# Performance work log

Measured on AMD Instinct MI355X. Metric: run time of the kernel, lower is better.

The kernel has to match this reference:

```python
import jax, jax.numpy as jnp
import numpy as np

B, N, E, C_IN, C_OUT = 16, 4096, 131072, 256, 256


def setup_inputs() -> dict:
    key = jax.random.key(0)
    k1, k2, k3, k4 = jax.random.split(key, 4)
    x = jax.random.normal(k1, (B, N, C_IN), dtype=jnp.float32)
    edge_index = jax.random.randint(k2, (B, 2, E), 0, N, dtype=jnp.int32)
    edge_weight = jax.random.uniform(k3, (B, E), dtype=jnp.float32)
    # glorot init for weight [C_in, C_out]
    scale = float(np.sqrt(6.0 / (C_IN + C_OUT)))
    W = jax.random.uniform(k4, (C_IN, C_OUT), dtype=jnp.float32, minval=-scale, maxval=scale)
    return {"x": x, "edge_index": edge_index, "edge_weight": edge_weight, "W": W}


def _gcn_one_graph(xi, ei, ewi, W):
    # xi: [N, C_in], ei: [2, E+N], ewi: [E+N]
    n = xi.shape[0]
    row, col = ei[0], ei[1]
    deg = jax.ops.segment_sum(ewi, row, num_segments=n)            # [N]
    deg_inv = jnp.where(deg > 0, jax.lax.rsqrt(deg), 0.0)          # deg^-0.5, inf -> 0
    norm = deg_inv[row] * ewi * deg_inv[col]                       # [E+N]
    xw = xi @ W                                                    # [N, C_out]
    msg = norm[:, None] * xw[col]                                  # gather + scale
    out = jax.ops.segment_sum(msg, row, num_segments=n)            # scatter-add to rows
    return jax.nn.relu(out)                                        # act = F.relu, bias=False


def reference(x, edge_index, edge_weight, W):
    b, n, _ = x.shape
    # add self loops with weight 1 (fill_value=1)
    loop = jnp.arange(n, dtype=edge_index.dtype)
    loop_idx = jnp.broadcast_to(jnp.stack([loop, loop])[None], (b, 2, n))
    ei = jnp.concatenate([edge_index, loop_idx], axis=-1)          # [B, 2, E+N]
    ew = jnp.concatenate([edge_weight, jnp.ones((b, n), x.dtype)], axis=-1)  # [B, E+N]
    return jax.vmap(_gcn_one_graph, in_axes=(0, 0, 0, None))(x, ei, ew, W)
```

## Files before the change

kernel.cpp:

```cpp
#include <hip/hip_runtime.h>
#include <cstdint>
#include <cstddef>

#define BB 16
#define NN 4096
#define EE 131072
#define CIN 256
#define COUT 256
#define NCH 16
#define CHE (EE / NCH)

typedef __attribute__((ext_vector_type(8))) _Float16 h16x8;
typedef __attribute__((ext_vector_type(4))) float f32x4;

#define GLDS16(g, l) __builtin_amdgcn_global_load_lds( \
    (const __attribute__((address_space(1))) uint32_t*)(g), \
    (__attribute__((address_space(3))) uint32_t*)(l), 16, 0, 0)

__global__ __launch_bounds__(256) void phaseA_kernel(const float* __restrict__ x, _Float16* __restrict__ xh,
                                                     const float* __restrict__ W, _Float16* __restrict__ wt,
                                                     const int* __restrict__ ei, const float* __restrict__ ew,
                                                     int* __restrict__ chist, float* __restrict__ wdeg) {
    __shared__ int h[NN];
    __shared__ float wh[NN];
    int bid = blockIdx.x;
    int tid = threadIdx.x;
    if (bid < BB * NCH) {
        int b = bid >> 4, c = bid & (NCH - 1);
        for (int i = tid; i < NN; i += 256) { h[i] = 0; wh[i] = 0.f; }
        __syncthreads();
        const int* rows = ei + (size_t)b * 2 * EE + (size_t)c * CHE;
        const float* w = ew + (size_t)b * EE + (size_t)c * CHE;
        #pragma unroll 4
        for (int j = 0; j < CHE / 256; ++j) {
            int row = rows[j * 256 + tid];
            float wv = w[j * 256 + tid];
            atomicAdd(&h[row], 1);
            atomicAdd(&wh[row], wv);
        }
        __syncthreads();
        int* co = chist + ((size_t)b * NCH + c) * NN;
        float* wo = wdeg + ((size_t)b * NCH + c) * NN;
        for (int i = tid; i < NN; i += 256) { co[i] = h[i]; wo[i] = wh[i]; }
    } else if (bid < BB * NCH + (BB * NN * CIN) / (256 * 8)) {
        size_t u = (size_t)(bid - BB * NCH) * 256 + tid;
        const float* g = &x[u * 8];
        float4 f0 = *reinterpret_cast<const float4*>(g);
        float4 f1 = *reinterpret_cast<const float4*>(g + 4);
        h16x8 v;
        v[0] = (_Float16)f0.x; v[1] = (_Float16)f0.y; v[2] = (_Float16)f0.z; v[3] = (_Float16)f0.w;
        v[4] = (_Float16)f1.x; v[5] = (_Float16)f1.y; v[6] = (_Float16)f1.z; v[7] = (_Float16)f1.w;
        *reinterpret_cast<h16x8*>(&xh[u * 8]) = v;
    } else {
        int n = bid - (BB * NCH + (BB * NN * CIN) / (256 * 8));
        int k = tid;
        wt[n * CIN + k] = (_Float16)W[(size_t)k * COUT + n];
    }
}

__global__ __launch_bounds__(1024) void scanfused_kernel(const int* __restrict__ chist, const float* __restrict__ wdeg,
                                                         int* __restrict__ chunkbase, int* __restrict__ roff,
                                                         float* __restrict__ dinv) {
    int b = blockIdx.x, tid = threadIdx.x;
    int wid = tid >> 6, lane = tid & 63;
    __shared__ int wsum[16];
    __shared__ int wbase[16];
    __shared__ int gtot_s;
    int carry = 0;
    for (int g = 0; g < 4; ++g) {
        int r = g * 1024 + tid;
        int cv[NCH];
        int tot = 0;
        float dsum = 1.0f;
        #pragma unroll
        for (int c = 0; c < NCH; ++c) {
            size_t idx = ((size_t)b * NCH + c) * NN + r;
            cv[c] = chist[idx];
            tot += cv[c];
            dsum += wdeg[idx];
        }
        dinv[b * NN + r] = rsqrtf(dsum);
        int incl = tot;
        #pragma unroll
        for (int off = 1; off < 64; off <<= 1) {
            int t = __shfl_up(incl, off, 64);
            if (lane >= off) incl += t;
        }
        if (lane == 63) wsum[wid] = incl;
        __syncthreads();
        if (wid == 0) {
            int v = (lane < 16) ? wsum[lane] : 0;
            int winc = v;
            #pragma unroll
            for (int off = 1; off < 16; off <<= 1) {
                int t = __shfl_up(winc, off, 64);
                if (lane >= off) winc += t;
            }
            if (lane < 16) wbase[lane] = winc - v;
            if (lane == 15) gtot_s = winc;
        }
        __syncthreads();
        int excl = carry + wbase[wid] + (incl - tot);
        roff[b * NN + r] = excl;
        int acc = excl;
        #pragma unroll
        for (int c = 0; c < NCH; ++c) {
            chunkbase[((size_t)b * NCH + c) * NN + r] = acc;
            acc += cv[c];
        }
        carry += gtot_s;
        __syncthreads();
    }
}

__global__ __launch_bounds__(256) void gemm_scatter_kernel(const _Float16* __restrict__ xh, const _Float16* __restrict__ wt,
                                                           _Float16* __restrict__ xw,
                                                           const int* __restrict__ ei, const float* __restrict__ ew,
                                                           const float* __restrict__ dinv, const int* __restrict__ chunkbase,
                                                           uint32_t* __restrict__ csr) {
    __shared__ __align__(16) char smem[32768];
    int bid = blockIdx.x;
    int tid = threadIdx.x;
    if (bid < 256) {
        int* basebuf = (int*)smem;
        float* dinvs = (float*)(smem + 16384);
        int b = bid >> 4, c = bid & (NCH - 1);
        for (int i = tid; i < NN; i += 256) {
            basebuf[i] = chunkbase[((size_t)b * NCH + c) * NN + i];
            dinvs[i] = dinv[b * NN + i];
        }
        __syncthreads();
        const int* rows = ei + (size_t)b * 2 * EE + (size_t)c * CHE;
        const int* cols = rows + EE;
        const float* w = ew + (size_t)b * EE + (size_t)c * CHE;
        uint32_t* cs = csr + (size_t)b * EE;
        #pragma unroll 4
        for (int jj = 0; jj < CHE / 256; ++jj) {
            int e = jj * 256 + tid;
            int row = rows[e];
            int col = cols[e];
            float nm = dinvs[row] * w[e] * dinvs[col];
            int pos = atomicAdd(&basebuf[row], 1);
            uint32_t nmh = (uint32_t)__builtin_bit_cast(unsigned short, (_Float16)nm);
            cs[pos] = ((uint32_t)col << 16) | nmh;
        }
    } else {
        _Float16* As = (_Float16*)smem;
        _Float16* Bs = As + 128 * 64;
        int g = bid - 256;
        int lane = tid & 63;
        int wave = tid >> 6;
        int bx = g >> 1, by = g & 1;
        int row0 = bx * 128, col0 = by * 128;
        int wr = wave >> 1, wc = wave & 1;
        int hi = lane >> 4, lo = lane & 15;
        int lr = lane >> 3, lk = (lane & 7) * 8;
        f32x4 acc[4][4] = {};

        for (int kk = 0; kk < CIN; kk += 64) {
            #pragma unroll
            for (int j = 0; j < 4; ++j) {
                int seg = j * 4 + wave;
                const _Float16* ga = &xh[(size_t)(row0 + seg * 8 + lr) * CIN + kk + lk];
                const _Float16* gb = &wt [(size_t)(col0 + seg * 8 + lr) * CIN + kk + lk];
                GLDS16(ga, &As[seg * 512]);
                GLDS16(gb, &Bs[seg * 512]);
            }
            __syncthreads();
            #pragma unroll
            for (int ks = 0; ks < 2; ++ks) {
                h16x8 a[4], b[4];
                #pragma unroll
                for (int m = 0; m < 4; ++m)
                    a[m] = *reinterpret_cast<const h16x8*>(&As[(wr * 64 + m * 16 + lo) * 64 + ks * 32 + 8 * hi]);
                #pragma unroll
                for (int n = 0; n < 4; ++n)
                    b[n] = *reinterpret_cast<const h16x8*>(&Bs[(wc * 64 + n * 16 + lo) * 64 + ks * 32 + 8 * hi]);
                #pragma unroll
                for (int m = 0; m < 4; ++m)
                    #pragma unroll
                    for (int n = 0; n < 4; ++n)
                        acc[m][n] = __builtin_amdgcn_mfma_f32_16x16x32_f16(a[m], b[n], acc[m][n], 0, 0, 0);
            }
            __syncthreads();
        }
        #pragma unroll
        for (int m = 0; m < 4; ++m)
            #pragma unroll
            for (int n = 0; n < 4; ++n)
                #pragma unroll
                for (int r = 0; r < 4; ++r) {
                    int row = row0 + wr * 64 + m * 16 + hi * 4 + r;
                    int col = col0 + wc * 64 + n * 16 + lo;
                    xw[(size_t)row * COUT + col] = (_Float16)acc[m][n][r];
                }
    }
}

#define MIXQLO(acc_, w_, qv_) asm("v_fma_mix_f32 %0, %1, %2, %0 op_sel:[0,0,0] op_sel_hi:[1,1,0]" \
                                  : "+v"(acc_) : "v"(w_), "v"(qv_));
#define MIXQHI(acc_, w_, qv_) asm("v_fma_mix_f32 %0, %1, %2, %0 op_sel:[1,0,0] op_sel_hi:[1,1,0]" \
                                  : "+v"(acc_) : "v"(w_), "v"(qv_));
#define ACCMIXQ(w_, qv_) { \
    MIXQLO(a0, (w_).x, qv_); MIXQHI(a1, (w_).x, qv_); \
    MIXQLO(a2, (w_).y, qv_); MIXQHI(a3, (w_).y, qv_); \
    MIXQLO(a4, (w_).z, qv_); MIXQHI(a5, (w_).z, qv_); \
    MIXQLO(a6, (w_).w, qv_); MIXQHI(a7, (w_).w, qv_); }
#define MIXSLO(acc_, w_, nm_) asm("v_fma_mix_f32 %0, %1, %2, %0 op_sel:[0,0,0] op_sel_hi:[1,0,0]" \
                                  : "+v"(acc_) : "v"(w_), "v"(nm_));
#define MIXSHI(acc_, w_, nm_) asm("v_fma_mix_f32 %0, %1, %2, %0 op_sel:[1,0,0] op_sel_hi:[1,0,0]" \
                                  : "+v"(acc_) : "v"(w_), "v"(nm_));

__global__ __launch_bounds__(256) void aggregate_kernel(const _Float16* __restrict__ xw, const float* __restrict__ dinv,
                                                        const int* __restrict__ roff, const uint32_t* __restrict__ csr,
                                                        float* __restrict__ out) {
    int bid = blockIdx.x;
    int xcd = bid & 7;
    int idx = bid >> 3;
    int b = xcd * 2 + (idx >> 10);
    int rowblk = idx & 1023;
    int wave = threadIdx.x >> 6;
    int lane = threadIdx.x & 63;
    int n = rowblk * 4 + wave;
    bool hiHalf = lane >= 32;
    int sub = lane & 31;
    uint32_t lanebyte = sub * 16;

    const int* rb = roff + b * NN;
    int s = __builtin_amdgcn_readfirstlane(rb[n]);
    int eRaw = (n == NN - 1) ? EE : rb[n + 1];
    int e = __builtin_amdgcn_readfirstlane(eRaw);
    int cnt = e - s;
    const uint32_t* cs = csr + (size_t)b * EE + s;

    const char* xwbase = (const char*)(xw + (size_t)b * NN * COUT);
    float a0 = 0.f, a1 = 0.f, a2 = 0.f, a3 = 0.f, a4 = 0.f, a5 = 0.f, a6 = 0.f, a7 = 0.f;

    {
        float di = dinv[b * NN + n];
        float sn = hiHalf ? 0.f : di * di;
        uint4 w = *reinterpret_cast<const uint4*>(xwbase + (size_t)n * (COUT * 2) + lanebyte);
        MIXSLO(a0, w.x, sn); MIXSHI(a1, w.x, sn);
        MIXSLO(a2, w.y, sn); MIXSHI(a3, w.y, sn);
        MIXSLO(a4, w.z, sn); MIXSHI(a5, w.z, sn);
        MIXSLO(a6, w.w, sn); MIXSHI(a7, w.w, sn);
    }

    int m = cnt & ~7;
    int i = 0;
    for (; i < m; i += 8) {
        uint32_t q[8];
        #pragma unroll
        for (int u = 0; u < 8; ++u) q[u] = cs[i + u];
        #pragma unroll
        for (int u = 0; u < 4; ++u) {
            uint32_t qv = hiHalf ? q[2 * u + 1] : q[2 * u];
            uint32_t offx = ((qv >> 16) << 9) + lanebyte;
            uint4 w = *reinterpret_cast<const uint4*>(xwbase + offx);
            ACCMIXQ(w, qv);
        }
    }
    if (i < cnt) {
        #pragma unroll
        for (int u = 0; u < 4; ++u) {
            int j0 = i + 2 * u, j1 = j0 + 1;
            uint32_t q0 = cs[(j0 < cnt) ? j0 : cnt - 1];
            uint32_t q1 = cs[(j1 < cnt) ? j1 : cnt - 1];
            if (j0 >= cnt) q0 &= 0xFFFF0000u;
            if (j1 >= cnt) q1 &= 0xFFFF0000u;
            uint32_t qv = hiHalf ? q1 : q0;
            uint32_t offx = ((qv >> 16) << 9) + lanebyte;
            uint4 w = *reinterpret_cast<const uint4*>(xwbase + offx);
            ACCMIXQ(w, qv);
        }
    }

    a0 += __shfl(a0, lane ^ 32, 64); a1 += __shfl(a1, lane ^ 32, 64);
    a2 += __shfl(a2, lane ^ 32, 64); a3 += __shfl(a3, lane ^ 32, 64);
    a4 += __shfl(a4, lane ^ 32, 64); a5 += __shfl(a5, lane ^ 32, 64);
    a6 += __shfl(a6, lane ^ 32, 64); a7 += __shfl(a7, lane ^ 32, 64);

    float4 o = hiHalf
        ? make_float4(fmaxf(a4, 0.f), fmaxf(a5, 0.f), fmaxf(a6, 0.f), fmaxf(a7, 0.f))
        : make_float4(fmaxf(a0, 0.f), fmaxf(a1, 0.f), fmaxf(a2, 0.f), fmaxf(a3, 0.f));
    float* orow = out + ((size_t)b * NN + n) * COUT + sub * 8 + (hiHalf ? 4 : 0);
    *reinterpret_cast<float4*>(orow) = o;
}

__global__ __launch_bounds__(256) void cvt_wt_kernel(const float* __restrict__ W, _Float16* __restrict__ wt) {
    int n = blockIdx.x;
    int k = threadIdx.x;
    wt[n * CIN + k] = (_Float16)W[(size_t)k * COUT + n];
}

__global__ __launch_bounds__(256) void init_deg_kernel(float* __restrict__ deg, float v) {
    int i = blockIdx.x * 256 + threadIdx.x;
    if (i < BB * NN) deg[i] = v;
}

__global__ __launch_bounds__(256) void deg_only_kernel(const int* __restrict__ ei, const float* __restrict__ ew,
                                                       float* __restrict__ deg) {
    int idx = blockIdx.x * 256 + threadIdx.x;
    if (idx >= BB * EE) return;
    int b = idx / EE, e = idx - b * EE;
    atomicAdd(&deg[b * NN + ei[(size_t)b * 2 * EE + e]], ew[(size_t)b * EE + e]);
}

__global__ __launch_bounds__(256) void deginv_kernel(const float* __restrict__ deg, float* __restrict__ dinv) {
    int i = blockIdx.x * 256 + threadIdx.x;
    if (i < BB * NN) {
        float d = deg[i];
        dinv[i] = (d > 0.0f) ? rsqrtf(d) : 0.0f;
    }
}

__global__ __launch_bounds__(256) void gemm_f32src_kernel(const float* __restrict__ x, const _Float16* __restrict__ wt,
                                                          _Float16* __restrict__ xw) {
    __shared__ _Float16 As[128][64];
    __shared__ _Float16 Bs[128][64];
    int tid = threadIdx.x;
    int lane = tid & 63;
    int wave = tid >> 6;
    int row0 = blockIdx.x * 128;
    int col0 = blockIdx.y * 128;
    int wr = wave >> 1, wc = wave & 1;
    int hi = lane >> 4, lo = lane & 15;
    f32x4 acc[4][4] = {};
    for (int kk = 0; kk < CIN; kk += 64) {
        #pragma unroll
        for (int j = 0; j < 4; ++j) {
            int c = j * 256 + tid;
            int r = c >> 3, kq = c & 7;
            const float* g = &x[(size_t)(row0 + r) * CIN + kk + 8 * kq];
            float4 f0 = *reinterpret_cast<const float4*>(g);
            float4 f1 = *reinterpret_cast<const float4*>(g + 4);
            h16x8 v;
            v[0] = (_Float16)f0.x; v[1] = (_Float16)f0.y; v[2] = (_Float16)f0.z; v[3] = (_Float16)f0.w;
            v[4] = (_Float16)f1.x; v[5] = (_Float16)f1.y; v[6] = (_Float16)f1.z; v[7] = (_Float16)f1.w;
            *reinterpret_cast<h16x8*>(&As[r][8 * kq]) = v;
        }
        #pragma unroll
        for (int j = 0; j < 4; ++j) {
            int c = j * 256 + tid;
            int r = c >> 3, kq = c & 7;
            *reinterpret_cast<h16x8*>(&Bs[r][8 * kq]) =
                *reinterpret_cast<const h16x8*>(&wt[(size_t)(col0 + r) * CIN + kk + 8 * kq]);
        }
        __syncthreads();
        #pragma unroll
        for (int ks = 0; ks < 2; ++ks) {
            h16x8 a[4], b[4];
            #pragma unroll
            for (int m = 0; m < 4; ++m)
                a[m] = *reinterpret_cast<const h16x8*>(&As[wr * 64 + m * 16 + lo][ks * 32 + 8 * hi]);
            #pragma unroll
            for (int n = 0; n < 4; ++n)
                b[n] = *reinterpret_cast<const h16x8*>(&Bs[wc * 64 + n * 16 + lo][ks * 32 + 8 * hi]);
            #pragma unroll
            for (int m = 0; m < 4; ++m)
                #pragma unroll
                for (int n = 0; n < 4; ++n)
                    acc[m][n] = __builtin_amdgcn_mfma_f32_16x16x32_f16(a[m], b[n], acc[m][n], 0, 0, 0);
        }
        __syncthreads();
    }
    #pragma unroll
    for (int m = 0; m < 4; ++m)
        #pragma unroll
        for (int n = 0; n < 4; ++n)
            #pragma unroll
            for (int r = 0; r < 4; ++r) {
                int row = row0 + wr * 64 + m * 16 + hi * 4 + r;
                int col = col0 + wc * 64 + n * 16 + lo;
                xw[(size_t)row * COUT + col] = (_Float16)acc[m][n][r];
            }
}

__global__ __launch_bounds__(256) void self_kernel(const _Float16* __restrict__ xw, const float* __restrict__ dinv,
                                                   float* __restrict__ out) {
    int bn = blockIdx.x;
    int c = threadIdx.x;
    float di = dinv[bn];
    out[(size_t)bn * COUT + c] = di * di * (float)xw[(size_t)bn * COUT + c];
}

__global__ __launch_bounds__(256) void scatter_atomic_kernel(const int* __restrict__ ei, const float* __restrict__ ew,
                                                             const float* __restrict__ dinv,
                                                             const _Float16* __restrict__ xw, float* __restrict__ out) {
    int be = blockIdx.x;
    int b = be / EE, e = be - b * EE;
    int c = threadIdx.x;
    int row = ei[(size_t)b * 2 * EE + e];
    int col = ei[(size_t)b * 2 * EE + EE + e];
    float w = ew[(size_t)b * EE + e];
    float nm = dinv[b * NN + row] * w * dinv[b * NN + col];
    const _Float16* xwb = xw + (size_t)b * NN * COUT;
    atomicAdd(&out[((size_t)b * NN + row) * COUT + c], nm * (float)xwb[(size_t)col * COUT + c]);
}

__global__ __launch_bounds__(256) void relu_kernel(float* __restrict__ out) {
    size_t i = (size_t)blockIdx.x * 256 + threadIdx.x;
    out[i] = fmaxf(out[i], 0.0f);
}

extern "C" void kernel_launch(void* const* d_in, const int* in_sizes, int n_in,
                              void* d_out, int out_size, void* d_ws, size_t ws_size,
                              hipStream_t stream) {
    const float* x  = (const float*)d_in[0];
    const int*   ei = (const int*)d_in[1];
    const float* ew = (const float*)d_in[2];
    const float* Wm = (const float*)d_in[3];
    float* out = (float*)d_out;

    char* ws = (char*)d_ws;
    size_t off = 0;
    auto alloc = [&](size_t bytes) -> void* {
        void* p = ws + off;
        off += (bytes + 255) & ~(size_t)255;
        return p;
    };
    _Float16* xw        = (_Float16*)alloc((size_t)BB * NN * COUT * 2);
    _Float16* xh        = (_Float16*)alloc((size_t)BB * NN * CIN * 2);
    int*      chist     = (int*)alloc((size_t)BB * NCH * NN * 4);
    float*    wdeg      = (float*)alloc((size_t)BB * NCH * NN * 4);
    int*      chunkbase = (int*)alloc((size_t)BB * NCH * NN * 4);
    int*      roff      = (int*)alloc((size_t)BB * NN * 4);
    float*    dinv      = (float*)alloc((size_t)BB * NN * 4);
    _Float16* wt        = (_Float16*)alloc((size_t)CIN * COUT * 2);
    uint32_t* csr       = (uint32_t*)chist;
    float*    deg_fb    = (float*)chist;
    bool use_csr = (ws_size >= off);

    if (use_csr) {
        const int xcvtBlocks = (BB * NN * CIN) / (256 * 8);
        phaseA_kernel<<<BB * NCH + xcvtBlocks + COUT, 256, 0, stream>>>(x, xh, Wm, wt, ei, ew, chist, wdeg);
        scanfused_kernel<<<BB, 1024, 0, stream>>>(chist, wdeg, chunkbase, roff, dinv);
        gemm_scatter_kernel<<<256 + (BB * NN / 128) * (COUT / 128), 256, 0, stream>>>(
            xh, wt, xw, ei, ew, dinv, chunkbase, csr);
        aggregate_kernel<<<BB * NN / 4, 256, 0, stream>>>(xw, dinv, roff, csr, out);
    } else {
        const int bnBlocks = (BB * NN) / 256;
        cvt_wt_kernel<<<COUT, CIN, 0, stream>>>(Wm, wt);
        init_deg_kernel<<<bnBlocks, 256, 0, stream>>>(deg_fb, 1.0f);
        deg_only_kernel<<<(BB * EE) / 256, 256, 0, stream>>>(ei, ew, deg_fb);
        deginv_kernel<<<bnBlocks, 256, 0, stream>>>(deg_fb, dinv);
        dim3 ggrid((BB * NN) / 128, COUT / 128);
        gemm_f32src_kernel<<<ggrid, 256, 0, stream>>>(x, wt, xw);
        self_kernel<<<BB * NN, 256, 0, stream>>>(xw, dinv, out);
        scatter_atomic_kernel<<<BB * EE, 256, 0, stream>>>(ei, ew, dinv, xw, out);
        relu_kernel<<<(BB * NN * COUT) / 256, 256, 0, stream>>>(out);
    }
}
```

Baseline: 135.1 us.

## Fuse fp32-to-fp16 conversion of x into GEMM and split scatter from GEMM

Drops the separate pass that converts x to fp16 into a workspace buffer. The GEMM now reads fp32 x directly and converts it while staging into LDS, which saves a full write and re-read of the fp16 copy. The combined gemm+scatter launch is split into two kernels, and the scatter uses an XCD-aware block-to-batch mapping. In exchange, the GEMM loses the async global_load_lds path and reads twice as many input bytes, and the scatter no longer runs concurrently with the GEMM.

```diff
diff --git a/kernel.cpp b/kernel.cpp
--- a/kernel.cpp
+++ b/kernel.cpp
@@ -13,12 +13,7 @@
 typedef __attribute__((ext_vector_type(8))) _Float16 h16x8;
 typedef __attribute__((ext_vector_type(4))) float f32x4;
 
-#define GLDS16(g, l) __builtin_amdgcn_global_load_lds( \
-    (const __attribute__((address_space(1))) uint32_t*)(g), \
-    (__attribute__((address_space(3))) uint32_t*)(l), 16, 0, 0)
-
-__global__ __launch_bounds__(256) void phaseA_kernel(const float* __restrict__ x, _Float16* __restrict__ xh,
-                                                     const float* __restrict__ W, _Float16* __restrict__ wt,
+__global__ __launch_bounds__(256) void phaseA_kernel(const float* __restrict__ W, _Float16* __restrict__ wt,
                                                      const int* __restrict__ ei, const float* __restrict__ ew,
                                                      int* __restrict__ chist, float* __restrict__ wdeg) {
     __shared__ int h[NN];
@@ -42,17 +37,8 @@
         int* co = chist + ((size_t)b * NCH + c) * NN;
         float* wo = wdeg + ((size_t)b * NCH + c) * NN;
         for (int i = tid; i < NN; i += 256) { co[i] = h[i]; wo[i] = wh[i]; }
-    } else if (bid < BB * NCH + (BB * NN * CIN) / (256 * 8)) {
-        size_t u = (size_t)(bid - BB * NCH) * 256 + tid;
-        const float* g = &x[u * 8];
-        float4 f0 = *reinterpret_cast<const float4*>(g);
-        float4 f1 = *reinterpret_cast<const float4*>(g + 4);
-        h16x8 v;
-        v[0] = (_Float16)f0.x; v[1] = (_Float16)f0.y; v[2] = (_Float16)f0.z; v[3] = (_Float16)f0.w;
-        v[4] = (_Float16)f1.x; v[5] = (_Float16)f1.y; v[6] = (_Float16)f1.z; v[7] = (_Float16)f1.w;
-        *reinterpret_cast<h16x8*>(&xh[u * 8]) = v;
     } else {
-        int n = bid - (BB * NCH + (BB * NN * CIN) / (256 * 8));
+        int n = bid - BB * NCH;
         int k = tid;
         wt[n * CIN + k] = (_Float16)W[(size_t)k * COUT + n];
     }
@@ -113,88 +99,98 @@
     }
 }
 
-__global__ __launch_bounds__(256) void gemm_scatter_kernel(const _Float16* __restrict__ xh, const _Float16* __restrict__ wt,
-                                                           _Float16* __restrict__ xw,
-                                                           const int* __restrict__ ei, const float* __restrict__ ew,
-                                                           const float* __restrict__ dinv, const int* __restrict__ chunkbase,
-                                                           uint32_t* __restrict__ csr) {
-    __shared__ __align__(16) char smem[32768];
+__global__ __launch_bounds__(256) void scatter2_kernel(const int* __restrict__ ei, const float* __restrict__ ew,
+                                                       const float* __restrict__ dinv, const int* __restrict__ chunkbase,
+                                                       uint32_t* __restrict__ csr) {
+    __shared__ int basebuf[NN];
+    __shared__ float dinvs[NN];
     int bid = blockIdx.x;
+    int xcd = bid & 7;
+    int j = bid >> 3;
+    int b = xcd * 2 + (j >> 4);
+    int c = j & (NCH - 1);
     int tid = threadIdx.x;
-    if (bid < 256) {
-        int* basebuf = (int*)smem;
-        float* dinvs = (float*)(smem + 16384);
-        int b = bid >> 4, c = bid & (NCH - 1);
-        for (int i = tid; i < NN; i += 256) {
-            basebuf[i] = chunkbase[((size_t)b * NCH + c) * NN + i];
-            dinvs[i] = dinv[b * NN + i];
-        }
-        __syncthreads();
-        const int* rows = ei + (size_t)b * 2 * EE + (size_t)c * CHE;
-        const int* cols = rows + EE;
-        const float* w = ew + (size_t)b * EE + (size_t)c * CHE;
-        uint32_t* cs = csr + (size_t)b * EE;
-        #pragma unroll 4
-        for (int jj = 0; jj < CHE / 256; ++jj) {
-            int e = jj * 256 + tid;
-            int row = rows[e];
-            int col = cols[e];
-            float nm = dinvs[row] * w[e] * dinvs[col];
-            int pos = atomicAdd(&basebuf[row], 1);
-            uint32_t nmh = (uint32_t)__builtin_bit_cast(unsigned short, (_Float16)nm);
-            cs[pos] = ((uint32_t)col << 16) | nmh;
-        }
-    } else {
-        _Float16* As = (_Float16*)smem;
-        _Float16* Bs = As + 128 * 64;
-        int g = bid - 256;
-        int lane = tid & 63;
-        int wave = tid >> 6;
-        int bx = g >> 1, by = g & 1;
-        int row0 = bx * 128, col0 = by * 128;
-        int wr = wave >> 1, wc = wave & 1;
-        int hi = lane >> 4, lo = lane & 15;
-        int lr = lane >> 3, lk = (lane & 7) * 8;
-        f32x4 acc[4][4] = {};
-
-        for (int kk = 0; kk < CIN; kk += 64) {
-            #pragma unroll
-            for (int j = 0; j < 4; ++j) {
-                int seg = j * 4 + wave;
-                const _Float16* ga = &xh[(size_t)(row0 + seg * 8 + lr) * CIN + kk + lk];
-                const _Float16* gb = &wt [(size_t)(col0 + seg * 8 + lr) * CIN + kk + lk];
-                GLDS16(ga, &As[seg * 512]);
-                GLDS16(gb, &Bs[seg * 512]);
-            }
-            __syncthreads();
-            #pragma unroll
-            for (int ks = 0; ks < 2; ++ks) {
-                h16x8 a[4], b[4];
-                #pragma unroll
-                for (int m = 0; m < 4; ++m)
-                    a[m] = *reinterpret_cast<const h16x8*>(&As[(wr * 64 + m * 16 + lo) * 64 + ks * 32 + 8 * hi]);
+    for (int i = tid; i < NN; i += 256) {
+        basebuf[i] = chunkbase[((size_t)b * NCH + c) * NN + i];
+        dinvs[i] = dinv[b * NN + i];
+    }
+    __syncthreads();
+    const int* rows = ei + (size_t)b * 2 * EE + (size_t)c * CHE;
+    const int* cols = rows + EE;
+    const float* w = ew + (size_t)b * EE + (size_t)c * CHE;
+    uint32_t* cs = csr + (size_t)b * EE;
+    #pragma unroll 4
+    for (int jj = 0; jj < CHE / 256; ++jj) {
+        int e = jj * 256 + tid;
+        int row = rows[e];
+        int col = cols[e];
+        float nm = dinvs[row] * w[e] * dinvs[col];
+        int pos = atomicAdd(&basebuf[row], 1);
+        uint32_t nmh = (uint32_t)__builtin_bit_cast(unsigned short, (_Float16)nm);
+        cs[pos] = ((uint32_t)col << 16) | nmh;
+    }
+}
+
+__global__ __launch_bounds__(256) void gemm_f32src_kernel(const float* __restrict__ x, const _Float16* __restrict__ wt,
+                                                          _Float16* __restrict__ xw) {
+    __shared__ _Float16 As[128][64];
+    __shared__ _Float16 Bs[128][64];
+    int tid = threadIdx.x;
+    int lane = tid & 63;
+    int wave = tid >> 6;
+    int row0 = blockIdx.x * 128;
+    int col0 = blockIdx.y * 128;
+    int wr = wave >> 1, wc = wave & 1;
+    int hi = lane >> 4, lo = lane & 15;
+    f32x4 acc[4][4] = {};
+    for (int kk = 0; kk < CIN; kk += 64) {
+        #pragma unroll
+        for (int j = 0; j < 4; ++j) {
+            int c = j * 256 + tid;
+            int r = c >> 3, kq = c & 7;
+            const float* g = &x[(size_t)(row0 + r) * CIN + kk + 8 * kq];
+            float4 f0 = *reinterpret_cast<const float4*>(g);
+            float4 f1 = *reinterpret_cast<const float4*>(g + 4);
+            h16x8 v;
+            v[0] = (_Float16)f0.x; v[1] = (_Float16)f0.y; v[2] = (_Float16)f0.z; v[3] = (_Float16)f0.w;
+            v[4] = (_Float16)f1.x; v[5] = (_Float16)f1.y; v[6] = (_Float16)f1.z; v[7] = (_Float16)f1.w;
+            *reinterpret_cast<h16x8*>(&As[r][8 * kq]) = v;
+        }
+        #pragma unroll
+        for (int j = 0; j < 4; ++j) {
+            int c = j * 256 + tid;
+            int r = c >> 3, kq = c & 7;
+            *reinterpret_cast<h16x8*>(&Bs[r][8 * kq]) =
+                *reinterpret_cast<const h16x8*>(&wt[(size_t)(col0 + r) * CIN + kk + 8 * kq]);
+        }
+        __syncthreads();
+        #pragma unroll
+        for (int ks = 0; ks < 2; ++ks) {
+            h16x8 a[4], b[4];
+            #pragma unroll
+            for (int m = 0; m < 4; ++m)
+                a[m] = *reinterpret_cast<const h16x8*>(&As[wr * 64 + m * 16 + lo][ks * 32 + 8 * hi]);
+            #pragma unroll
+            for (int n = 0; n < 4; ++n)
+                b[n] = *reinterpret_cast<const h16x8*>(&Bs[wc * 64 + n * 16 + lo][ks * 32 + 8 * hi]);
+            #pragma unroll
+            for (int m = 0; m < 4; ++m)
                 #pragma unroll
                 for (int n = 0; n < 4; ++n)
-                    b[n] = *reinterpret_cast<const h16x8*>(&Bs[(wc * 64 + n * 16 + lo) * 64 + ks * 32 + 8 * hi]);
-                #pragma unroll
-                for (int m = 0; m < 4; ++m)
-                    #pragma unroll
-                    for (int n = 0; n < 4; ++n)
-                        acc[m][n] = __builtin_amdgcn_mfma_f32_16x16x32_f16(a[m], b[n], acc[m][n], 0, 0, 0);
+                    acc[m][n] = __builtin_amdgcn_mfma_f32_16x16x32_f16(a[m], b[n], acc[m][n], 0, 0, 0);
+        }
+        __syncthreads();
+    }
+    #pragma unroll
+    for (int m = 0; m < 4; ++m)
+        #pragma unroll
+        for (int n = 0; n < 4; ++n)
+            #pragma unroll
+            for (int r = 0; r < 4; ++r) {
+                int row = row0 + wr * 64 + m * 16 + hi * 4 + r;
+                int col = col0 + wc * 64 + n * 16 + lo;
+                xw[(size_t)row * COUT + col] = (_Float16)acc[m][n][r];
             }
-            __syncthreads();
-        }
-        #pragma unroll
-        for (int m = 0; m < 4; ++m)
-            #pragma unroll
-            for (int n = 0; n < 4; ++n)
-                #pragma unroll
-                for (int r = 0; r < 4; ++r) {
-                    int row = row0 + wr * 64 + m * 16 + hi * 4 + r;
-                    int col = col0 + wc * 64 + n * 16 + lo;
-                    xw[(size_t)row * COUT + col] = (_Float16)acc[m][n][r];
-                }
-    }
 }
 
 #define MIXQLO(acc_, w_, qv_) asm("v_fma_mix_f32 %0, %1, %2, %0 op_sel:[0,0,0] op_sel_hi:[1,1,0]" \
@@ -314,68 +310,6 @@
     }
 }
 
-__global__ __launch_bounds__(256) void gemm_f32src_kernel(const float* __restrict__ x, const _Float16* __restrict__ wt,
-                                                          _Float16* __restrict__ xw) {
-    __shared__ _Float16 As[128][64];
-    __shared__ _Float16 Bs[128][64];
-    int tid = threadIdx.x;
-    int lane = tid & 63;
-    int wave = tid >> 6;
-    int row0 = blockIdx.x * 128;
-    int col0 = blockIdx.y * 128;
-    int wr = wave >> 1, wc = wave & 1;
-    int hi = lane >> 4, lo = lane & 15;
-    f32x4 acc[4][4] = {};
-    for (int kk = 0; kk < CIN; kk += 64) {
-        #pragma unroll
-        for (int j = 0; j < 4; ++j) {
-            int c = j * 256 + tid;
-            int r = c >> 3, kq = c & 7;
-            const float* g = &x[(size_t)(row0 + r) * CIN + kk + 8 * kq];
-            float4 f0 = *reinterpret_cast<const float4*>(g);
-            float4 f1 = *reinterpret_cast<const float4*>(g + 4);
-            h16x8 v;
-            v[0] = (_Float16)f0.x; v[1] = (_Float16)f0.y; v[2] = (_Float16)f0.z; v[3] = (_Float16)f0.w;
-            v[4] = (_Float16)f1.x; v[5] = (_Float16)f1.y; v[6] = (_Float16)f1.z; v[7] = (_Float16)f1.w;
-            *reinterpret_cast<h16x8*>(&As[r][8 * kq]) = v;
-        }
-        #pragma unroll
-        for (int j = 0; j < 4; ++j) {
-            int c = j * 256 + tid;
-            int r = c >> 3, kq = c & 7;
-            *reinterpret_cast<h16x8*>(&Bs[r][8 * kq]) =
-                *reinterpret_cast<const h16x8*>(&wt[(size_t)(col0 + r) * CIN + kk + 8 * kq]);
-        }
-        __syncthreads();
-        #pragma unroll
-        for (int ks = 0; ks < 2; ++ks) {
-            h16x8 a[4], b[4];
-            #pragma unroll
-            for (int m = 0; m < 4; ++m)
-                a[m] = *reinterpret_cast<const h16x8*>(&As[wr * 64 + m * 16 + lo][ks * 32 + 8 * hi]);
-            #pragma unroll
-            for (int n = 0; n < 4; ++n)
-                b[n] = *reinterpret_cast<const h16x8*>(&Bs[wc * 64 + n * 16 + lo][ks * 32 + 8 * hi]);
-            #pragma unroll
-            for (int m = 0; m < 4; ++m)
-                #pragma unroll
-                for (int n = 0; n < 4; ++n)
-                    acc[m][n] = __builtin_amdgcn_mfma_f32_16x16x32_f16(a[m], b[n], acc[m][n], 0, 0, 0);
-        }
-        __syncthreads();
-    }
-    #pragma unroll
-    for (int m = 0; m < 4; ++m)
-        #pragma unroll
-        for (int n = 0; n < 4; ++n)
-            #pragma unroll
-            for (int r = 0; r < 4; ++r) {
-                int row = row0 + wr * 64 + m * 16 + hi * 4 + r;
-                int col = col0 + wc * 64 + n * 16 + lo;
-                xw[(size_t)row * COUT + col] = (_Float16)acc[m][n][r];
-            }
-}
-
 __global__ __launch_bounds__(256) void self_kernel(const _Float16* __restrict__ xw, const float* __restrict__ dinv,
                                                    float* __restrict__ out) {
     int bn = blockIdx.x;
@@ -420,7 +354,6 @@
         return p;
     };
     _Float16* xw        = (_Float16*)alloc((size_t)BB * NN * COUT * 2);
-    _Float16* xh        = (_Float16*)alloc((size_t)BB * NN * CIN * 2);
     int*      chist     = (int*)alloc((size_t)BB * NCH * NN * 4);
     float*    wdeg      = (float*)alloc((size_t)BB * NCH * NN * 4);
     int*      chunkbase = (int*)alloc((size_t)BB * NCH * NN * 4);
@@ -432,11 +365,11 @@
     bool use_csr = (ws_size >= off);
 
     if (use_csr) {
-        const int xcvtBlocks = (BB * NN * CIN) / (256 * 8);
-        phaseA_kernel<<<BB * NCH + xcvtBlocks + COUT, 256, 0, stream>>>(x, xh, Wm, wt, ei, ew, chist, wdeg);
+        phaseA_kernel<<<BB * NCH + COUT, 256, 0, stream>>>(Wm, wt, ei, ew, chist, wdeg);
         scanfused_kernel<<<BB, 1024, 0, stream>>>(chist, wdeg, chunkbase, roff, dinv);
-        gemm_scatter_kernel<<<256 + (BB * NN / 128) * (COUT / 128), 256, 0, stream>>>(
-            xh, wt, xw, ei, ew, dinv, chunkbase, csr);
+        scatter2_kernel<<<BB * NCH, 256, 0, stream>>>(ei, ew, dinv, chunkbase, csr);
+        dim3 ggrid((BB * NN) / 128, COUT / 128);
+        gemm_f32src_kernel<<<ggrid, 256, 0, stream>>>(x, wt, xw);
         aggregate_kernel<<<BB * NN / 4, 256, 0, stream>>>(xw, dinv, roff, csr, out);
     } else {
         const int bnBlocks = (BB * NN) / 256;
```

Result: no change. 133.4 us (-1.2%).
